# Performance work log

Hardware: AMD Instinct MI355X
Metric: run time of the kernel (lower is better)

The kernel has to match this reference:

```python
import jax, jax.numpy as jnp
import numpy as np

N = 100000
E = 3200000
F_IN, H1, H2, C = 128, 64, 32, 10


def setup_inputs() -> dict:
    key = jax.random.key(0)
    ks = jax.random.split(key, 8)
    x = jax.random.normal(ks[0], (N, F_IN), dtype=jnp.float32)
    edge_index = jax.random.randint(ks[1], (2, E), 0, N, dtype=jnp.int64)
    W1 = jax.random.normal(ks[2], (F_IN, H1), dtype=jnp.float32) / np.sqrt(F_IN)
    b1 = jnp.zeros((H1,), dtype=jnp.float32)
    W2 = jax.random.normal(ks[3], (H1, H2), dtype=jnp.float32) / np.sqrt(H1)
    b2 = jnp.zeros((H2,), dtype=jnp.float32)
    Wc = jax.random.normal(ks[4], (H2, C), dtype=jnp.float32) / np.sqrt(H2)
    bc = jnp.zeros((C,), dtype=jnp.float32)
    return {"x": x, "edge_index": edge_index, "W1": W1, "b1": b1,
            "W2": W2, "b2": b2, "Wc": Wc, "bc": bc}


def gcn_conv(x, src, dst, W, b, n):
    # PyG GCNConv: x' = D^{-1/2} (A + I) D^{-1/2} (X W) + b
    h = x @ W                                        # [N, H]
    ones = jnp.ones((src.shape[0],), dtype=h.dtype)
    deg = jax.ops.segment_sum(ones, dst, num_segments=n) + 1.0  # +1 self loop
    dinv = jax.lax.rsqrt(deg)                        # deg >= 1, safe
    norm = dinv[src] * dinv[dst]                     # [E]
    msg = h[src] * norm[:, None]                     # [E, H] gather + scale
    agg = jax.ops.segment_sum(msg, dst, num_segments=n)
    # self-loop contribution: norm_ii = 1/deg_i
    out = agg + h * (dinv * dinv)[:, None]
    return out + b


def reference(x, edge_index, W1, b1, W2, b2, Wc, bc):
    n = x.shape[0]
    src, dst = edge_index[0], edge_index[1]
    h = gcn_conv(x, src, dst, W1, b1, n)
    h = jax.nn.relu(h)
    # dropout is identity in eval mode (training=False)
    h = gcn_conv(h, src, dst, W2, b2, n)
    h = jax.nn.relu(h)
    logits = h @ Wc + bc
    return jax.nn.log_softmax(logits, axis=1)
```

## Files before the change

### kernel.cpp

```cpp
#include <hip/hip_runtime.h>


#define BSHIFT 8
#define BMASK 255
#define NBUCK_MAX 512
#define TILE 4096
#define EPT 16

__device__ __forceinline__ unsigned pack_bf16(float lo, float hi) {
    unsigned ul = __float_as_uint(lo);
    ul = (ul + 0x7FFFu + ((ul >> 16) & 1u)) >> 16;
    unsigned uh = __float_as_uint(hi);
    uh = ((uh + 0x7FFFu + ((uh >> 16) & 1u)) >> 16) << 16;
    return ul | uh;
}

__global__ void k_hist(const int* __restrict__ dst, int* __restrict__ bcnt, int E) {
    __shared__ int h[NBUCK_MAX];
    for (int i = threadIdx.x; i < NBUCK_MAX; i += blockDim.x) h[i] = 0;
    __syncthreads();
    for (int e = blockIdx.x * blockDim.x + threadIdx.x; e < E; e += gridDim.x * blockDim.x)
        atomicAdd(&h[dst[e] >> BSHIFT], 1);
    __syncthreads();
    for (int i = threadIdx.x; i < NBUCK_MAX; i += blockDim.x)
        if (h[i]) atomicAdd(&bcnt[i], h[i]);
}

__global__ void k_scanb(const int* __restrict__ bcnt, int* __restrict__ bbase,
                        int* __restrict__ gcur, int E) {
    __shared__ int s[NBUCK_MAX];
    int t = threadIdx.x;
    int v = bcnt[t];
    s[t] = v;
    __syncthreads();
    for (int o = 1; o < NBUCK_MAX; o <<= 1) {
        int u = (t >= o) ? s[t - o] : 0;
        __syncthreads();
        s[t] += u;
        __syncthreads();
    }
    int ex = s[t] - v;
    bbase[t] = ex;
    gcur[t] = ex;
    if (t == NBUCK_MAX - 1) bbase[NBUCK_MAX] = E;
}

__global__ __launch_bounds__(256) void k_binA(const int* __restrict__ src,
                                              const int* __restrict__ dst,
                                              int* __restrict__ gcur,
                                              int* __restrict__ binned, int E) {
    __shared__ int hist[NBUCK_MAX];
    __shared__ int lbase[NBUCK_MAX];
    __shared__ int gdelta[NBUCK_MAX];
    __shared__ int cnt2[NBUCK_MAX];
    __shared__ int scanb[256];
    __shared__ int stage[TILE];
    __shared__ unsigned short sbucket[TILE];

    int t = threadIdx.x;
    for (int i = t; i < NBUCK_MAX; i += 256) { hist[i] = 0; cnt2[i] = 0; }
    __syncthreads();

    int tileStart = blockIdx.x * TILE;
    int cntTile = min(TILE, E - tileStart);

    int vals[EPT];
    int bks[EPT];
#pragma unroll
    for (int i = 0; i < EPT; i++) {
        int e = tileStart + t + i * 256;
        if (e < E) {
            int s = src[e], d = dst[e];
            vals[i] = s | ((d & BMASK) << 17);
            bks[i] = d >> BSHIFT;
            atomicAdd(&hist[bks[i]], 1);
        } else bks[i] = -1;
    }
    __syncthreads();

    int a0 = hist[2 * t], a1 = hist[2 * t + 1];
    int ts = a0 + a1;
    scanb[t] = ts;
    __syncthreads();
    for (int o = 1; o < 256; o <<= 1) {
        int u = (t >= o) ? scanb[t - o] : 0;
        __syncthreads();
        scanb[t] += u;
        __syncthreads();
    }
    int ex = scanb[t] - ts;
    lbase[2 * t] = ex;
    lbase[2 * t + 1] = ex + a0;
    __syncthreads();

    for (int b = t; b < NBUCK_MAX; b += 256) {
        int c = hist[b];
        int g = c ? atomicAdd(&gcur[b], c) : 0;
        gdelta[b] = g - lbase[b];
    }
#pragma unroll
    for (int i = 0; i < EPT; i++) {
        if (bks[i] >= 0) {
            int rr = atomicAdd(&cnt2[bks[i]], 1);
            int slot = lbase[bks[i]] + rr;
            stage[slot] = vals[i];
            sbucket[slot] = (unsigned short)bks[i];
        }
    }
    __syncthreads();
    for (int i = t; i < cntTile; i += 256) {
        int b = sbucket[i];
        binned[gdelta[b] + i] = stage[i];
    }
}

__global__ void k_sortcsr(const int* __restrict__ bbase, const int* __restrict__ binned,
                          int* __restrict__ rowptr, float* __restrict__ dinv,
                          int* __restrict__ csr, int n, int E) {
    __shared__ int cnt[256];
    __shared__ int sc[256];
    __shared__ int rpl[256];
    __shared__ int lcur[256];
    int b = blockIdx.x, t = threadIdx.x;
    cnt[t] = 0; lcur[t] = 0;
    __syncthreads();
    int beg = bbase[b], end = bbase[b + 1];
    for (int i = beg + t; i < end; i += 256)
        atomicAdd(&cnt[(binned[i] >> 17) & BMASK], 1);
    __syncthreads();
    int v = cnt[t];
    sc[t] = v;
    __syncthreads();
    for (int o = 1; o < 256; o <<= 1) {
        int u = (t >= o) ? sc[t - o] : 0;
        __syncthreads();
        sc[t] += u;
        __syncthreads();
    }
    int rp = beg + sc[t] - v;
    rpl[t] = rp;
    int g = (b << BSHIFT) + t;
    if (g < n) {
        rowptr[g] = rp;
        dinv[g] = rsqrtf((float)v + 1.0f);
        if (g == n - 1) rowptr[n] = E;
    }
    __syncthreads();
    for (int i = beg + t; i < end; i += 256) {
        int vv = binned[i];
        int ln = (vv >> 17) & BMASK;
        int k = atomicAdd(&lcur[ln], 1);
        csr[rpl[ln] + k] = vv & 0x1FFFF;
    }
}

template<int K, int M, int R>
__global__ __launch_bounds__(256) void k_gemm(const float* __restrict__ X,
                                              const float* __restrict__ W,
                                              const float* __restrict__ dinv,
                                              unsigned* __restrict__ hsb, int n) {
    constexpr int MW = M / 4;
    __shared__ float Ws[K * M];
    for (int i = threadIdx.x; i < K * M; i += 256) Ws[i] = W[i];
    __syncthreads();
    int w = threadIdx.x >> 6, lane = threadIdx.x & 63;
    int wo = w * MW;
    int r0 = blockIdx.x * (64 * R) + lane;
    float acc[R][MW];
#pragma unroll
    for (int i = 0; i < R; i++)
#pragma unroll
        for (int j = 0; j < MW; j++) acc[i][j] = 0.f;

    for (int k = 0; k < K; k += 4) {
        float4 xv[R];
#pragma unroll
        for (int i = 0; i < R; i++) {
            int rr = r0 + 64 * i;
            xv[i] = (rr < n) ? *(const float4*)(X + (size_t)rr * K + k)
                             : make_float4(0.f, 0.f, 0.f, 0.f);
        }
#pragma unroll
        for (int kk = 0; kk < 4; kk++) {
#pragma unroll
            for (int j = 0; j < MW; j += 4) {
                float4 wv = *(const float4*)&Ws[(k + kk) * M + wo + j];
#pragma unroll
                for (int i = 0; i < R; i++) {
                    float xs = (kk == 0) ? xv[i].x : (kk == 1) ? xv[i].y
                             : (kk == 2) ? xv[i].z : xv[i].w;
                    acc[i][j + 0] += xs * wv.x;
                    acc[i][j + 1] += xs * wv.y;
                    acc[i][j + 2] += xs * wv.z;
                    acc[i][j + 3] += xs * wv.w;
                }
            }
        }
    }
#pragma unroll
    for (int i = 0; i < R; i++) {
        int rr = r0 + 64 * i;
        if (rr < n) {
            float di = dinv[rr];
            unsigned p[MW / 2];
#pragma unroll
            for (int jj = 0; jj < MW / 2; jj++)
                p[jj] = pack_bf16(acc[i][2 * jj] * di, acc[i][2 * jj + 1] * di);
            unsigned* hr = hsb + (size_t)rr * (M / 2) + wo / 2;
#pragma unroll
            for (int jj = 0; jj < MW / 2; jj += 4)
                *(uint4*)(hr + jj) = make_uint4(p[jj], p[jj + 1], p[jj + 2], p[jj + 3]);
        }
    }
}

__global__ void k_agg64n(const int* __restrict__ rowptr, const int* __restrict__ csr,
                         const uint4* __restrict__ hsb, const float* __restrict__ dinv,
                         const float* __restrict__ bv, float* __restrict__ out, int n) {
    __shared__ float bs[64];
    if (threadIdx.x < 64) bs[threadIdx.x] = bv[threadIdx.x];
    __syncthreads();
    int d = (blockIdx.x * blockDim.x + threadIdx.x) >> 6;
    if (d >= n) return;
    int lane = threadIdx.x & 63;
    int q = lane >> 3;
    int r = lane & 7;
    int beg = rowptr[d], end = rowptr[d + 1];
    float acc[8];
#pragma unroll
    for (int i = 0; i < 8; i++) acc[i] = 0.f;
    int base = beg;
    for (; base + 16 <= end; base += 16) {
        int sA = csr[base + q];
        int sB = csr[base + 8 + q];
        uint4 wA = hsb[(size_t)sA * 8 + r];
        uint4 wB = hsb[(size_t)sB * 8 + r];
        acc[0] += __uint_as_float(wA.x << 16);  acc[1] += __uint_as_float(wA.x & 0xFFFF0000u);
        acc[2] += __uint_as_float(wA.y << 16);  acc[3] += __uint_as_float(wA.y & 0xFFFF0000u);
        acc[4] += __uint_as_float(wA.z << 16);  acc[5] += __uint_as_float(wA.z & 0xFFFF0000u);
        acc[6] += __uint_as_float(wA.w << 16);  acc[7] += __uint_as_float(wA.w & 0xFFFF0000u);
        acc[0] += __uint_as_float(wB.x << 16);  acc[1] += __uint_as_float(wB.x & 0xFFFF0000u);
        acc[2] += __uint_as_float(wB.y << 16);  acc[3] += __uint_as_float(wB.y & 0xFFFF0000u);
        acc[4] += __uint_as_float(wB.z << 16);  acc[5] += __uint_as_float(wB.z & 0xFFFF0000u);
        acc[6] += __uint_as_float(wB.w << 16);  acc[7] += __uint_as_float(wB.w & 0xFFFF0000u);
    }
    if (base + q < end) {
        uint4 w = hsb[(size_t)csr[base + q] * 8 + r];
        acc[0] += __uint_as_float(w.x << 16);  acc[1] += __uint_as_float(w.x & 0xFFFF0000u);
        acc[2] += __uint_as_float(w.y << 16);  acc[3] += __uint_as_float(w.y & 0xFFFF0000u);
        acc[4] += __uint_as_float(w.z << 16);  acc[5] += __uint_as_float(w.z & 0xFFFF0000u);
        acc[6] += __uint_as_float(w.w << 16);  acc[7] += __uint_as_float(w.w & 0xFFFF0000u);
    }
    if (base + 8 + q < end) {
        uint4 w = hsb[(size_t)csr[base + 8 + q] * 8 + r];
        acc[0] += __uint_as_float(w.x << 16);  acc[1] += __uint_as_float(w.x & 0xFFFF0000u);
        acc[2] += __uint_as_float(w.y << 16);  acc[3] += __uint_as_float(w.y & 0xFFFF0000u);
        acc[4] += __uint_as_float(w.z << 16);  acc[5] += __uint_as_float(w.z & 0xFFFF0000u);
        acc[6] += __uint_as_float(w.w << 16);  acc[7] += __uint_as_float(w.w & 0xFFFF0000u);
    }
#pragma unroll
    for (int i = 0; i < 8; i++) {
        acc[i] += __shfl_xor(acc[i], 8, 64);
        acc[i] += __shfl_xor(acc[i], 16, 64);
        acc[i] += __shfl_xor(acc[i], 32, 64);
    }
    uint4 ws = hsb[(size_t)d * 8 + r];
    acc[0] += __uint_as_float(ws.x << 16);  acc[1] += __uint_as_float(ws.x & 0xFFFF0000u);
    acc[2] += __uint_as_float(ws.y << 16);  acc[3] += __uint_as_float(ws.y & 0xFFFF0000u);
    acc[4] += __uint_as_float(ws.z << 16);  acc[5] += __uint_as_float(ws.z & 0xFFFF0000u);
    acc[6] += __uint_as_float(ws.w << 16);  acc[7] += __uint_as_float(ws.w & 0xFFFF0000u);
    if (q == 0) {
        float di = dinv[d];
        float v[8];
#pragma unroll
        for (int i = 0; i < 8; i++) v[i] = fmaxf(acc[i] * di + bs[8 * r + i], 0.f);
        float* o = out + (size_t)d * 64 + 8 * r;
        *(float4*)(o + 0) = make_float4(v[0], v[1], v[2], v[3]);
        *(float4*)(o + 4) = make_float4(v[4], v[5], v[6], v[7]);
    }
}

__global__ void k_agg32n(const int* __restrict__ rowptr, const int* __restrict__ csr,
                         const uint4* __restrict__ hsb, const float* __restrict__ dinv,
                         const float* __restrict__ bv, float* __restrict__ out, int n) {
    __shared__ float bs[32];
    if (threadIdx.x < 32) bs[threadIdx.x] = bv[threadIdx.x];
    __syncthreads();
    int d = (blockIdx.x * blockDim.x + threadIdx.x) >> 6;
    if (d >= n) return;
    int lane = threadIdx.x & 63;
    int q = lane >> 2;
    int r = lane & 3;
    int beg = rowptr[d], end = rowptr[d + 1];
    float acc[8];
#pragma unroll
    for (int i = 0; i < 8; i++) acc[i] = 0.f;
    int base = beg;
    for (; base + 32 <= end; base += 32) {
        int sA = csr[base + q];
        int sB = csr[base + 16 + q];
        uint4 wA = hsb[(size_t)sA * 4 + r];
        uint4 wB = hsb[(size_t)sB * 4 + r];
        acc[0] += __uint_as_float(wA.x << 16);  acc[1] += __uint_as_float(wA.x & 0xFFFF0000u);
        acc[2] += __uint_as_float(wA.y << 16);  acc[3] += __uint_as_float(wA.y & 0xFFFF0000u);
        acc[4] += __uint_as_float(wA.z << 16);  acc[5] += __uint_as_float(wA.z & 0xFFFF0000u);
        acc[6] += __uint_as_float(wA.w << 16);  acc[7] += __uint_as_float(wA.w & 0xFFFF0000u);
        acc[0] += __uint_as_float(wB.x << 16);  acc[1] += __uint_as_float(wB.x & 0xFFFF0000u);
        acc[2] += __uint_as_float(wB.y << 16);  acc[3] += __uint_as_float(wB.y & 0xFFFF0000u);
        acc[4] += __uint_as_float(wB.z << 16);  acc[5] += __uint_as_float(wB.z & 0xFFFF0000u);
        acc[6] += __uint_as_float(wB.w << 16);  acc[7] += __uint_as_float(wB.w & 0xFFFF0000u);
    }
    if (base + q < end) {
        uint4 w = hsb[(size_t)csr[base + q] * 4 + r];
        acc[0] += __uint_as_float(w.x << 16);  acc[1] += __uint_as_float(w.x & 0xFFFF0000u);
        acc[2] += __uint_as_float(w.y << 16);  acc[3] += __uint_as_float(w.y & 0xFFFF0000u);
        acc[4] += __uint_as_float(w.z << 16);  acc[5] += __uint_as_float(w.z & 0xFFFF0000u);
        acc[6] += __uint_as_float(w.w << 16);  acc[7] += __uint_as_float(w.w & 0xFFFF0000u);
    }
    if (base + 16 + q < end) {
        uint4 w = hsb[(size_t)csr[base + 16 + q] * 4 + r];
        acc[0] += __uint_as_float(w.x << 16);  acc[1] += __uint_as_float(w.x & 0xFFFF0000u);
        acc[2] += __uint_as_float(w.y << 16);  acc[3] += __uint_as_float(w.y & 0xFFFF0000u);
        acc[4] += __uint_as_float(w.z << 16);  acc[5] += __uint_as_float(w.z & 0xFFFF0000u);
        acc[6] += __uint_as_float(w.w << 16);  acc[7] += __uint_as_float(w.w & 0xFFFF0000u);
    }
#pragma unroll
    for (int i = 0; i < 8; i++) {
        acc[i] += __shfl_xor(acc[i], 4, 64);
        acc[i] += __shfl_xor(acc[i], 8, 64);
        acc[i] += __shfl_xor(acc[i], 16, 64);
        acc[i] += __shfl_xor(acc[i], 32, 64);
    }
    uint4 ws = hsb[(size_t)d * 4 + r];
    acc[0] += __uint_as_float(ws.x << 16);  acc[1] += __uint_as_float(ws.x & 0xFFFF0000u);
    acc[2] += __uint_as_float(ws.y << 16);  acc[3] += __uint_as_float(ws.y & 0xFFFF0000u);
    acc[4] += __uint_as_float(ws.z << 16);  acc[5] += __uint_as_float(ws.z & 0xFFFF0000u);
    acc[6] += __uint_as_float(ws.w << 16);  acc[7] += __uint_as_float(ws.w & 0xFFFF0000u);
    if (q == 0) {
        float di = dinv[d];
        float v[8];
#pragma unroll
        for (int i = 0; i < 8; i++) v[i] = fmaxf(acc[i] * di + bs[8 * r + i], 0.f);
        float* o = out + (size_t)d * 32 + 8 * r;
        *(float4*)(o + 0) = make_float4(v[0], v[1], v[2], v[3]);
        *(float4*)(o + 4) = make_float4(v[4], v[5], v[6], v[7]);
    }
}

__global__ void k_classifier(const float* __restrict__ ACT, const float* __restrict__ Wc,
                             const float* __restrict__ bc, float* __restrict__ out, int n) {
    __shared__ float Wcs[32 * 10];
    __shared__ float bcs[10];
    for (int i = threadIdx.x; i < 320; i += blockDim.x) Wcs[i] = Wc[i];
    if (threadIdx.x < 10) bcs[threadIdx.x] = bc[threadIdx.x];
    __syncthreads();
    int r = blockIdx.x * blockDim.x + threadIdx.x;
    if (r >= n) return;
    const float* a = ACT + (size_t)r * 32;
    float logits[10];
#pragma unroll
    for (int c = 0; c < 10; c++) logits[c] = bcs[c];
#pragma unroll
    for (int k = 0; k < 32; k += 4) {
        float4 av = *(const float4*)(a + k);
#pragma unroll
        for (int c = 0; c < 10; c++) {
            logits[c] += av.x * Wcs[(k + 0) * 10 + c] + av.y * Wcs[(k + 1) * 10 + c]
                       + av.z * Wcs[(k + 2) * 10 + c] + av.w * Wcs[(k + 3) * 10 + c];
        }
    }
    float m = logits[0];
#pragma unroll
    for (int c = 1; c < 10; c++) m = fmaxf(m, logits[c]);
    float ssum = 0.f;
#pragma unroll
    for (int c = 0; c < 10; c++) ssum += __expf(logits[c] - m);
    float lse = m + __logf(ssum);
    float* o = out + (size_t)r * 10;
#pragma unroll
    for (int c = 0; c < 10; c++) o[c] = logits[c] - lse;
}

extern "C" void kernel_launch(void* const* d_in, const int* in_sizes, int n_in,
                              void* d_out, int out_size, void* d_ws, size_t ws_size,
                              hipStream_t stream) {
    const float* x  = (const float*)d_in[0];
    const int*   ei = (const int*)d_in[1];
    const float* W1 = (const float*)d_in[2];
    const float* b1 = (const float*)d_in[3];
    const float* W2 = (const float*)d_in[4];
    const float* b2 = (const float*)d_in[5];
    const float* Wc = (const float*)d_in[6];
    const float* bc = (const float*)d_in[7];
    float* out = (float*)d_out;

    const int N = in_sizes[0] / 128;
    const int E = in_sizes[1] / 2;
    const int* src = ei;
    const int* dst = ei + E;

    const int NBUCK = (N + BMASK) >> BSHIFT;
    const int NTILE = (E + TILE - 1) / TILE;

    char* ws = (char*)d_ws;
    size_t off = 0;
    auto alloc = [&](size_t elems) {
        void* p = ws + off;
        off += ((elems * 4 + 1023) & ~(size_t)1023);
        return p;
    };
    float*    dinv   = (float*)alloc(N);
    int*      bcnt   = (int*)alloc(NBUCK_MAX);
    int*      bbase  = (int*)alloc(NBUCK_MAX + 1);
    int*      gcur   = (int*)alloc(NBUCK_MAX);
    int*      rowptr = (int*)alloc(N + 1);
    int*      binned = (int*)alloc(E);
    int*      csr    = (int*)alloc(E);
    unsigned* hsb    = (unsigned*)alloc((size_t)N * 32);
    float*    act    = (float*)alloc((size_t)N * 64);

    hipMemsetAsync(bcnt, 0, sizeof(int) * NBUCK_MAX, stream);

    k_hist<<<512, 256, 0, stream>>>(dst, bcnt, E);
    k_scanb<<<1, NBUCK_MAX, 0, stream>>>(bcnt, bbase, gcur, E);
    k_binA<<<NTILE, 256, 0, stream>>>(src, dst, gcur, binned, E);
    k_sortcsr<<<NBUCK, 256, 0, stream>>>(bbase, binned, rowptr, dinv, csr, N, E);

    k_gemm<128, 64, 2><<<(N + 127) / 128, 256, 0, stream>>>(x, W1, dinv, hsb, N);
    k_agg64n<<<(N * 64 + 255) / 256, 256, 0, stream>>>(rowptr, csr, (const uint4*)hsb,
                                                       dinv, b1, act, N);

    k_gemm<64, 32, 4><<<(N + 255) / 256, 256, 0, stream>>>(act, W2, dinv, hsb, N);
    k_agg32n<<<(N * 64 + 255) / 256, 256, 0, stream>>>(rowptr, csr, (const uint4*)hsb,
                                                       dinv, b2, act, N);

    k_classifier<<<(N + 255) / 256, 256, 0, stream>>>(act, Wc, bc, out, N);
}
```

Baseline: 366.5 us.

## Fuse layer-2 GEMM into layer-1 aggregation and classifier into layer-2 aggregation

After: 363.0 us. About the same (-1.0%).

```diff
diff --git a/kernel.cpp b/kernel.cpp
--- a/kernel.cpp
+++ b/kernel.cpp
@@ -6,6 +6,7 @@
 #define NBUCK_MAX 512
 #define TILE 4096
 #define EPT 16
+#define NPW 4
 
 __device__ __forceinline__ unsigned pack_bf16(float lo, float hi) {
     unsigned ul = __float_as_uint(lo);
@@ -214,171 +215,158 @@
     }
 }
 
-__global__ void k_agg64n(const int* __restrict__ rowptr, const int* __restrict__ csr,
-                         const uint4* __restrict__ hsb, const float* __restrict__ dinv,
-                         const float* __restrict__ bv, float* __restrict__ out, int n) {
-    __shared__ float bs[64];
-    if (threadIdx.x < 64) bs[threadIdx.x] = bv[threadIdx.x];
-    __syncthreads();
-    int d = (blockIdx.x * blockDim.x + threadIdx.x) >> 6;
-    if (d >= n) return;
+#define ACC8(V) \
+    acc[0] += __uint_as_float((V).x << 16);  acc[1] += __uint_as_float((V).x & 0xFFFF0000u); \
+    acc[2] += __uint_as_float((V).y << 16);  acc[3] += __uint_as_float((V).y & 0xFFFF0000u); \
+    acc[4] += __uint_as_float((V).z << 16);  acc[5] += __uint_as_float((V).z & 0xFFFF0000u); \
+    acc[6] += __uint_as_float((V).w << 16);  acc[7] += __uint_as_float((V).w & 0xFFFF0000u);
+
+__global__ __launch_bounds__(256) void k_agg64f(
+        const int* __restrict__ rowptr, const int* __restrict__ csr,
+        const uint4* __restrict__ hsb, const float* __restrict__ dinv,
+        const float* __restrict__ b1, const float* __restrict__ W2,
+        unsigned* __restrict__ hsb2, int n) {
+    int wid = (blockIdx.x * blockDim.x + threadIdx.x) >> 6;
     int lane = threadIdx.x & 63;
-    int q = lane >> 3;
-    int r = lane & 7;
-    int beg = rowptr[d], end = rowptr[d + 1];
-    float acc[8];
-#pragma unroll
-    for (int i = 0; i < 8; i++) acc[i] = 0.f;
-    int base = beg;
-    for (; base + 16 <= end; base += 16) {
-        int sA = csr[base + q];
-        int sB = csr[base + 8 + q];
-        uint4 wA = hsb[(size_t)sA * 8 + r];
-        uint4 wB = hsb[(size_t)sB * 8 + r];
-        acc[0] += __uint_as_float(wA.x << 16);  acc[1] += __uint_as_float(wA.x & 0xFFFF0000u);
-        acc[2] += __uint_as_float(wA.y << 16);  acc[3] += __uint_as_float(wA.y & 0xFFFF0000u);
-        acc[4] += __uint_as_float(wA.z << 16);  acc[5] += __uint_as_float(wA.z & 0xFFFF0000u);
-        acc[6] += __uint_as_float(wA.w << 16);  acc[7] += __uint_as_float(wA.w & 0xFFFF0000u);
-        acc[0] += __uint_as_float(wB.x << 16);  acc[1] += __uint_as_float(wB.x & 0xFFFF0000u);
-        acc[2] += __uint_as_float(wB.y << 16);  acc[3] += __uint_as_float(wB.y & 0xFFFF0000u);
-        acc[4] += __uint_as_float(wB.z << 16);  acc[5] += __uint_as_float(wB.z & 0xFFFF0000u);
-        acc[6] += __uint_as_float(wB.w << 16);  acc[7] += __uint_as_float(wB.w & 0xFFFF0000u);
-    }
-    if (base + q < end) {
-        uint4 w = hsb[(size_t)csr[base + q] * 8 + r];
-        acc[0] += __uint_as_float(w.x << 16);  acc[1] += __uint_as_float(w.x & 0xFFFF0000u);
-        acc[2] += __uint_as_float(w.y << 16);  acc[3] += __uint_as_float(w.y & 0xFFFF0000u);
-        acc[4] += __uint_as_float(w.z << 16);  acc[5] += __uint_as_float(w.z & 0xFFFF0000u);
-        acc[6] += __uint_as_float(w.w << 16);  acc[7] += __uint_as_float(w.w & 0xFFFF0000u);
-    }
-    if (base + 8 + q < end) {
-        uint4 w = hsb[(size_t)csr[base + 8 + q] * 8 + r];
-        acc[0] += __uint_as_float(w.x << 16);  acc[1] += __uint_as_float(w.x & 0xFFFF0000u);
-        acc[2] += __uint_as_float(w.y << 16);  acc[3] += __uint_as_float(w.y & 0xFFFF0000u);
-        acc[4] += __uint_as_float(w.z << 16);  acc[5] += __uint_as_float(w.z & 0xFFFF0000u);
-        acc[6] += __uint_as_float(w.w << 16);  acc[7] += __uint_as_float(w.w & 0xFFFF0000u);
-    }
+    int q = lane >> 3, r = lane & 7;
+    int d0 = wid * NPW;
+    if (d0 >= n) return;
+    float w2r[8][4];
+    float b1r[8];
 #pragma unroll
     for (int i = 0; i < 8; i++) {
-        acc[i] += __shfl_xor(acc[i], 8, 64);
-        acc[i] += __shfl_xor(acc[i], 16, 64);
-        acc[i] += __shfl_xor(acc[i], 32, 64);
-    }
-    uint4 ws = hsb[(size_t)d * 8 + r];
-    acc[0] += __uint_as_float(ws.x << 16);  acc[1] += __uint_as_float(ws.x & 0xFFFF0000u);
-    acc[2] += __uint_as_float(ws.y << 16);  acc[3] += __uint_as_float(ws.y & 0xFFFF0000u);
-    acc[4] += __uint_as_float(ws.z << 16);  acc[5] += __uint_as_float(ws.z & 0xFFFF0000u);
-    acc[6] += __uint_as_float(ws.w << 16);  acc[7] += __uint_as_float(ws.w & 0xFFFF0000u);
-    if (q == 0) {
+        b1r[i] = b1[8 * r + i];
+#pragma unroll
+        for (int jj = 0; jj < 4; jj++)
+            w2r[i][jj] = W2[(8 * r + i) * 32 + 4 * q + jj];
+    }
+    int dend = min(d0 + NPW, n);
+    for (int d = d0; d < dend; d++) {
+        int beg = rowptr[d], end = rowptr[d + 1];
+        float acc[8];
+#pragma unroll
+        for (int i = 0; i < 8; i++) acc[i] = 0.f;
+        int base = beg;
+        for (; base + 16 <= end; base += 16) {
+            int sA = csr[base + q];
+            int sB = csr[base + 8 + q];
+            uint4 wA = hsb[(size_t)sA * 8 + r];
+            uint4 wB = hsb[(size_t)sB * 8 + r];
+            ACC8(wA)
+            ACC8(wB)
+        }
+        if (base + q < end) {
+            uint4 wv = hsb[(size_t)csr[base + q] * 8 + r];
+            ACC8(wv)
+        }
+        if (base + 8 + q < end) {
+            uint4 wv = hsb[(size_t)csr[base + 8 + q] * 8 + r];
+            ACC8(wv)
+        }
+#pragma unroll
+        for (int i = 0; i < 8; i++) {
+            acc[i] += __shfl_xor(acc[i], 8, 64);
+            acc[i] += __shfl_xor(acc[i], 16, 64);
+            acc[i] += __shfl_xor(acc[i], 32, 64);
+        }
+        uint4 wsf = hsb[(size_t)d * 8 + r];
+        ACC8(wsf)
         float di = dinv[d];
         float v[8];
 #pragma unroll
-        for (int i = 0; i < 8; i++) v[i] = fmaxf(acc[i] * di + bs[8 * r + i], 0.f);
-        float* o = out + (size_t)d * 64 + 8 * r;
-        *(float4*)(o + 0) = make_float4(v[0], v[1], v[2], v[3]);
-        *(float4*)(o + 4) = make_float4(v[4], v[5], v[6], v[7]);
-    }
-}
-
-__global__ void k_agg32n(const int* __restrict__ rowptr, const int* __restrict__ csr,
-                         const uint4* __restrict__ hsb, const float* __restrict__ dinv,
-                         const float* __restrict__ bv, float* __restrict__ out, int n) {
-    __shared__ float bs[32];
-    if (threadIdx.x < 32) bs[threadIdx.x] = bv[threadIdx.x];
-    __syncthreads();
-    int d = (blockIdx.x * blockDim.x + threadIdx.x) >> 6;
-    if (d >= n) return;
+        for (int i = 0; i < 8; i++) v[i] = fmaxf(acc[i] * di + b1r[i], 0.f);
+        float h[4] = {0.f, 0.f, 0.f, 0.f};
+#pragma unroll
+        for (int i = 0; i < 8; i++)
+#pragma unroll
+            for (int jj = 0; jj < 4; jj++) h[jj] += v[i] * w2r[i][jj];
+#pragma unroll
+        for (int jj = 0; jj < 4; jj++) {
+            h[jj] += __shfl_xor(h[jj], 1, 64);
+            h[jj] += __shfl_xor(h[jj], 2, 64);
+            h[jj] += __shfl_xor(h[jj], 4, 64);
+        }
+        if (r == 0) {
+            unsigned p0 = pack_bf16(h[0] * di, h[1] * di);
+            unsigned p1 = pack_bf16(h[2] * di, h[3] * di);
+            *(uint2*)(hsb2 + (size_t)d * 16 + 2 * q) = make_uint2(p0, p1);
+        }
+    }
+}
+
+__global__ __launch_bounds__(256) void k_agg32f(
+        const int* __restrict__ rowptr, const int* __restrict__ csr,
+        const uint4* __restrict__ hsb2, const float* __restrict__ dinv,
+        const float* __restrict__ b2, const float* __restrict__ Wc,
+        const float* __restrict__ bc, float* __restrict__ out, int n) {
+    int wid = (blockIdx.x * blockDim.x + threadIdx.x) >> 6;
     int lane = threadIdx.x & 63;
-    int q = lane >> 2;
-    int r = lane & 3;
-    int beg = rowptr[d], end = rowptr[d + 1];
-    float acc[8];
-#pragma unroll
-    for (int i = 0; i < 8; i++) acc[i] = 0.f;
-    int base = beg;
-    for (; base + 32 <= end; base += 32) {
-        int sA = csr[base + q];
-        int sB = csr[base + 16 + q];
-        uint4 wA = hsb[(size_t)sA * 4 + r];
-        uint4 wB = hsb[(size_t)sB * 4 + r];
-        acc[0] += __uint_as_float(wA.x << 16);  acc[1] += __uint_as_float(wA.x & 0xFFFF0000u);
-        acc[2] += __uint_as_float(wA.y << 16);  acc[3] += __uint_as_float(wA.y & 0xFFFF0000u);
-        acc[4] += __uint_as_float(wA.z << 16);  acc[5] += __uint_as_float(wA.z & 0xFFFF0000u);
-        acc[6] += __uint_as_float(wA.w << 16);  acc[7] += __uint_as_float(wA.w & 0xFFFF0000u);
-        acc[0] += __uint_as_float(wB.x << 16);  acc[1] += __uint_as_float(wB.x & 0xFFFF0000u);
-        acc[2] += __uint_as_float(wB.y << 16);  acc[3] += __uint_as_float(wB.y & 0xFFFF0000u);
-        acc[4] += __uint_as_float(wB.z << 16);  acc[5] += __uint_as_float(wB.z & 0xFFFF0000u);
-        acc[6] += __uint_as_float(wB.w << 16);  acc[7] += __uint_as_float(wB.w & 0xFFFF0000u);
-    }
-    if (base + q < end) {
-        uint4 w = hsb[(size_t)csr[base + q] * 4 + r];
-        acc[0] += __uint_as_float(w.x << 16);  acc[1] += __uint_as_float(w.x & 0xFFFF0000u);
-        acc[2] += __uint_as_float(w.y << 16);  acc[3] += __uint_as_float(w.y & 0xFFFF0000u);
-        acc[4] += __uint_as_float(w.z << 16);  acc[5] += __uint_as_float(w.z & 0xFFFF0000u);
-        acc[6] += __uint_as_float(w.w << 16);  acc[7] += __uint_as_float(w.w & 0xFFFF0000u);
-    }
-    if (base + 16 + q < end) {
-        uint4 w = hsb[(size_t)csr[base + 16 + q] * 4 + r];
-        acc[0] += __uint_as_float(w.x << 16);  acc[1] += __uint_as_float(w.x & 0xFFFF0000u);
-        acc[2] += __uint_as_float(w.y << 16);  acc[3] += __uint_as_float(w.y & 0xFFFF0000u);
-        acc[4] += __uint_as_float(w.z << 16);  acc[5] += __uint_as_float(w.z & 0xFFFF0000u);
-        acc[6] += __uint_as_float(w.w << 16);  acc[7] += __uint_as_float(w.w & 0xFFFF0000u);
-    }
+    int q = lane >> 2, r = lane & 3;
+    int d0 = wid * NPW;
+    if (d0 >= n) return;
+    float wcr[8];
+    float b2r[8];
+    float bcr = (q < 10) ? bc[q] : 0.f;
 #pragma unroll
     for (int i = 0; i < 8; i++) {
-        acc[i] += __shfl_xor(acc[i], 4, 64);
-        acc[i] += __shfl_xor(acc[i], 8, 64);
-        acc[i] += __shfl_xor(acc[i], 16, 64);
-        acc[i] += __shfl_xor(acc[i], 32, 64);
-    }
-    uint4 ws = hsb[(size_t)d * 4 + r];
-    acc[0] += __uint_as_float(ws.x << 16);  acc[1] += __uint_as_float(ws.x & 0xFFFF0000u);
-    acc[2] += __uint_as_float(ws.y << 16);  acc[3] += __uint_as_float(ws.y & 0xFFFF0000u);
-    acc[4] += __uint_as_float(ws.z << 16);  acc[5] += __uint_as_float(ws.z & 0xFFFF0000u);
-    acc[6] += __uint_as_float(ws.w << 16);  acc[7] += __uint_as_float(ws.w & 0xFFFF0000u);
-    if (q == 0) {
+        b2r[i] = b2[8 * r + i];
+        wcr[i] = (q < 10) ? Wc[(8 * r + i) * 10 + q] : 0.f;
+    }
+    int dend = min(d0 + NPW, n);
+    for (int d = d0; d < dend; d++) {
+        int beg = rowptr[d], end = rowptr[d + 1];
+        float acc[8];
+#pragma unroll
+        for (int i = 0; i < 8; i++) acc[i] = 0.f;
+        int base = beg;
+        for (; base + 32 <= end; base += 32) {
+            int sA = csr[base + q];
+            int sB = csr[base + 16 + q];
+            uint4 wA = hsb2[(size_t)sA * 4 + r];
+            uint4 wB = hsb2[(size_t)sB * 4 + r];
+            ACC8(wA)
+            ACC8(wB)
+        }
+        if (base + q < end) {
+            uint4 wv = hsb2[(size_t)csr[base + q] * 4 + r];
+            ACC8(wv)
+        }
+        if (base + 16 + q < end) {
+            uint4 wv = hsb2[(size_t)csr[base + 16 + q] * 4 + r];
+            ACC8(wv)
+        }
+#pragma unroll
+        for (int i = 0; i < 8; i++) {
+            acc[i] += __shfl_xor(acc[i], 4, 64);
+            acc[i] += __shfl_xor(acc[i], 8, 64);
+            acc[i] += __shfl_xor(acc[i], 16, 64);
+            acc[i] += __shfl_xor(acc[i], 32, 64);
+        }
+        uint4 wsf = hsb2[(size_t)d * 4 + r];
+        ACC8(wsf)
         float di = dinv[d];
-        float v[8];
-#pragma unroll
-        for (int i = 0; i < 8; i++) v[i] = fmaxf(acc[i] * di + bs[8 * r + i], 0.f);
-        float* o = out + (size_t)d * 32 + 8 * r;
-        *(float4*)(o + 0) = make_float4(v[0], v[1], v[2], v[3]);
-        *(float4*)(o + 4) = make_float4(v[4], v[5], v[6], v[7]);
-    }
-}
-
-__global__ void k_classifier(const float* __restrict__ ACT, const float* __restrict__ Wc,
-                             const float* __restrict__ bc, float* __restrict__ out, int n) {
-    __shared__ float Wcs[32 * 10];
-    __shared__ float bcs[10];
-    for (int i = threadIdx.x; i < 320; i += blockDim.x) Wcs[i] = Wc[i];
-    if (threadIdx.x < 10) bcs[threadIdx.x] = bc[threadIdx.x];
-    __syncthreads();
-    int r = blockIdx.x * blockDim.x + threadIdx.x;
-    if (r >= n) return;
-    const float* a = ACT + (size_t)r * 32;
-    float logits[10];
-#pragma unroll
-    for (int c = 0; c < 10; c++) logits[c] = bcs[c];
-#pragma unroll
-    for (int k = 0; k < 32; k += 4) {
-        float4 av = *(const float4*)(a + k);
+        float part = 0.f;
+#pragma unroll
+        for (int i = 0; i < 8; i++) {
+            float v = fmaxf(acc[i] * di + b2r[i], 0.f);
+            part += v * wcr[i];
+        }
+        part += __shfl_xor(part, 1, 64);
+        part += __shfl_xor(part, 2, 64);
+        float mylogit = part + bcr;
+        float m = -1e30f;
+        float l[10];
 #pragma unroll
         for (int c = 0; c < 10; c++) {
-            logits[c] += av.x * Wcs[(k + 0) * 10 + c] + av.y * Wcs[(k + 1) * 10 + c]
-                       + av.z * Wcs[(k + 2) * 10 + c] + av.w * Wcs[(k + 3) * 10 + c];
-        }
-    }
-    float m = logits[0];
-#pragma unroll
-    for (int c = 1; c < 10; c++) m = fmaxf(m, logits[c]);
-    float ssum = 0.f;
-#pragma unroll
-    for (int c = 0; c < 10; c++) ssum += __expf(logits[c] - m);
-    float lse = m + __logf(ssum);
-    float* o = out + (size_t)r * 10;
-#pragma unroll
-    for (int c = 0; c < 10; c++) o[c] = logits[c] - lse;
+            l[c] = __shfl(mylogit, 4 * c, 64);
+            m = fmaxf(m, l[c]);
+        }
+        float ssum = 0.f;
+#pragma unroll
+        for (int c = 0; c < 10; c++) ssum += __expf(l[c] - m);
+        float lse = m + __logf(ssum);
+        if (r == 0 && q < 10) out[(size_t)d * 10 + q] = mylogit - lse;
+    }
 }
 
 extern "C" void kernel_launch(void* const* d_in, const int* in_sizes, int n_in,
@@ -401,6 +389,7 @@
 
     const int NBUCK = (N + BMASK) >> BSHIFT;
     const int NTILE = (E + TILE - 1) / TILE;
+    const int NW = (N + NPW - 1) / NPW;
 
     char* ws = (char*)d_ws;
     size_t off = 0;
@@ -417,7 +406,7 @@
     int*      binned = (int*)alloc(E);
     int*      csr    = (int*)alloc(E);
     unsigned* hsb    = (unsigned*)alloc((size_t)N * 32);
-    float*    act    = (float*)alloc((size_t)N * 64);
+    unsigned* hsb2   = (unsigned*)alloc((size_t)N * 16);
 
     hipMemsetAsync(bcnt, 0, sizeof(int) * NBUCK_MAX, stream);
 
@@ -427,12 +416,8 @@
     k_sortcsr<<<NBUCK, 256, 0, stream>>>(bbase, binned, rowptr, dinv, csr, N, E);
 
     k_gemm<128, 64, 2><<<(N + 127) / 128, 256, 0, stream>>>(x, W1, dinv, hsb, N);
-    k_agg64n<<<(N * 64 + 255) / 256, 256, 0, stream>>>(rowptr, csr, (const uint4*)hsb,
-                                                       dinv, b1, act, N);
-
-    k_gemm<64, 32, 4><<<(N + 255) / 256, 256, 0, stream>>>(act, W2, dinv, hsb, N);
-    k_agg32n<<<(N * 64 + 255) / 256, 256, 0, stream>>>(rowptr, csr, (const uint4*)hsb,
-                                                       dinv, b2, act, N);
-
-    k_classifier<<<(N + 255) / 256, 256, 0, stream>>>(act, Wc, bc, out, N);
-}
+    k_agg64f<<<(NW * 64 + 255) / 256, 256, 0, stream>>>(rowptr, csr, (const uint4*)hsb,
+                                                        dinv, b1, W2, hsb2, N);
+    k_agg32f<<<(NW * 64 + 255) / 256, 256, 0, stream>>>(rowptr, csr, (const uint4*)hsb2,
+                                                        dinv, b2, Wc, bc, out, N);
+}
```
